# Kernel optimization log

Hardware: AMD Instinct MI355X
Metric: run time of the kernel (lower is better)

## Reference

```python
import jax, jax.numpy as jnp
import numpy as np

BS, VARNUM, EMB_DIM, SEED_DIM, N_HEADS = 32, 16384, 128, 128, 16


def setup_inputs() -> dict:
    key = jax.random.key(0)
    k1, k2, k3, k4 = jax.random.split(key, 4)
    query_seed = jax.random.normal(k1, (BS, SEED_DIM), dtype=jnp.float32)
    embeddings = jax.random.normal(k2, (BS, VARNUM, EMB_DIM), dtype=jnp.float32)
    # mask over varnum//2 base variables; 1 = keep, 0 = mask out
    attn_mask = jax.random.randint(k3, (BS, VARNUM // 2), 0, 2, dtype=jnp.int32)
    # xavier_normal_ init: std = sqrt(2 / (fan_in + fan_out))
    xavier_std = float(np.sqrt(2.0 / (EMB_DIM + SEED_DIM)))
    w_qs = jax.random.normal(k4, (N_HEADS, EMB_DIM, SEED_DIM), dtype=jnp.float32) * xavier_std
    return {"query_seed": query_seed, "embeddings": embeddings,
            "attn_mask": attn_mask, "w_qs": w_qs}


def _l2_normalize(x):
    # x / ||x||_2 along last dim (no eps, matching torch source)
    return x / jnp.linalg.norm(x, axis=-1, keepdims=True)


def reference(query_seed, embeddings, attn_mask, w_qs):
    bs, varnum, emb_dim = embeddings.shape
    n_heads = w_qs.shape[0]

    norm_embs = _l2_normalize(embeddings)                      # [bs, varnum, emb]
    # mm(w_qs.view(-1, seed), seed.T).T.view(bs, n_heads, emb) == einsum
    qs = jnp.tanh(jnp.einsum("hes,bs->bhe", w_qs, query_seed))  # [bs, heads, emb]
    norm_qs = _l2_normalize(qs)

    # orthogonality loss between head queries
    gram = jnp.einsum("bhe,bge->bhg", norm_qs, norm_qs)        # [bs, h, h]
    diff = gram - jnp.eye(n_heads, dtype=gram.dtype)
    loss = jnp.sum(diff * diff) / bs

    # cosine-similarity attention
    attn = jnp.einsum("bhe,bve->bhv", norm_qs, norm_embs)      # [bs, h, varnum]
    mask_full = jnp.concatenate([attn_mask, attn_mask], axis=1)[:, None, :]  # [bs,1,varnum]
    attn = jnp.where(mask_full == 0, -jnp.inf, attn)
    final_attn = jax.nn.softmax(attn, axis=-1)
    rc = jnp.einsum("bhv,bve->bhe", final_attn, embeddings)    # values = embeddings
    return rc, loss
```

## Files before the change

### kernel.cpp

```cpp
#include <hip/hip_runtime.h>
#include <hip/hip_bf16.h>
#include <cstdint>

#define BS     32
#define VARNUM 16384
#define EMB    128
#define SEEDD  128
#define NH     16
#define HALFV  8192

#define NCHUNK 32
#define VT     (VARNUM / NCHUNK)
#define TV     64
#define NTILE  (VT / TV)

#define EST 2080
#define PST 144

#define OFF_NORMQ 0
#define SZ_NORMQ  (BS*NH*EMB*4)
#define OFF_LOSSP (OFF_NORMQ + SZ_NORMQ)
#define SZ_LOSSP  256
#define OFF_LPART (OFF_LOSSP + SZ_LOSSP)
#define SZ_LPART  (BS*NCHUNK*NH*4)
#define OFF_PACC  (OFF_LPART + SZ_LPART)
#define SZ_PACC   ((size_t)BS*NCHUNK*NH*EMB*4)

typedef __attribute__((ext_vector_type(8))) short bf16x8;
typedef __attribute__((ext_vector_type(4))) float f32x4;

static __device__ __forceinline__ uint16_t f2bf(float f) {
    uint32_t u = __float_as_uint(f);
    return (uint16_t)((u + 0x7FFFu + ((u >> 16) & 1u)) >> 16);
}
static __device__ __forceinline__ uint32_t packbf(float a, float b) {
    __hip_bfloat162 h = __float22bfloat162_rn(make_float2(a, b));
    uint32_t u;
    __builtin_memcpy(&u, &h, 4);
    return u;
}
static __device__ __forceinline__ float dot4(float4 a, float4 b) {
    return a.x*b.x + a.y*b.y + a.z*b.z + a.w*b.w;
}

__global__ __launch_bounds__(128) void k1_q(const float* __restrict__ seed,
                                            const float* __restrict__ wqs,
                                            float* __restrict__ normq) {
    const int bh = blockIdx.x;
    const int b = bh >> 4, h = bh & 15;
    const int e = threadIdx.x;
    __shared__ __align__(16) float s_seed[SEEDD];
    s_seed[e] = seed[b*SEEDD + e];
    __syncthreads();
    const float4* w4 = (const float4*)(wqs + ((size_t)(h*EMB + e))*SEEDD);
    const float4* s4 = (const float4*)s_seed;
    float acc = 0.f;
    #pragma unroll
    for (int j = 0; j < SEEDD/4; ++j) acc += dot4(w4[j], s4[j]);
    float t = tanhf(acc);
    float sq = t*t;
    #pragma unroll
    for (int off = 32; off; off >>= 1) sq += __shfl_xor(sq, off);
    __shared__ float s_part[2];
    if ((threadIdx.x & 63) == 0) s_part[threadIdx.x >> 6] = sq;
    __syncthreads();
    float tot = s_part[0] + s_part[1];
    normq[((size_t)b*NH + h)*EMB + e] = t * rsqrtf(tot);
}

__global__ __launch_bounds__(256) void k2_loss(const float* __restrict__ normq,
                                               float* __restrict__ lossp) {
    const int b = blockIdx.x;
    const int h = threadIdx.x >> 4, g = threadIdx.x & 15;
    const float4* qh = (const float4*)(normq + ((size_t)b*NH + h)*EMB);
    const float4* qg = (const float4*)(normq + ((size_t)b*NH + g)*EMB);
    float d = 0.f;
    #pragma unroll
    for (int j = 0; j < EMB/4; ++j) d += dot4(qh[j], qg[j]);
    d -= (h == g) ? 1.f : 0.f;
    float sq = d*d;
    #pragma unroll
    for (int off = 32; off; off >>= 1) sq += __shfl_xor(sq, off);
    __shared__ float sp[4];
    if ((threadIdx.x & 63) == 0) sp[threadIdx.x >> 6] = sq;
    __syncthreads();
    if (threadIdx.x == 0) lossp[b] = sp[0] + sp[1] + sp[2] + sp[3];
}

__global__ __launch_bounds__(256, 4) void k_fused(const float* __restrict__ emb,
                                                  const int* __restrict__ mask,
                                                  const float* __restrict__ normq,
                                                  float* __restrict__ pacc,
                                                  float* __restrict__ lpart) {
    const int chunk = blockIdx.x, b = blockIdx.y;
    const int tid = threadIdx.x;
    const int w   = tid >> 6;
    const int l   = tid & 63;
    const int lhi = l >> 4;
    const int llo = l & 15;

    __shared__ __align__(16) unsigned char Elds[8*EST];
    __shared__ __align__(16) unsigned char Plds[16*PST];
    __shared__ __align__(16) float nsq[TV];
    __shared__ float lred[4][NH];

    bf16x8 qf[4];
    {
        const float* qrow = normq + ((size_t)b*NH + llo)*EMB;
        #pragma unroll
        for (int f = 0; f < 4; ++f) {
            const float4* qs = (const float4*)(qrow + f*32 + lhi*8);
            float4 a = qs[0], c = qs[1];
            bf16x8 t;
            t[0]=(short)f2bf(a.x); t[1]=(short)f2bf(a.y); t[2]=(short)f2bf(a.z); t[3]=(short)f2bf(a.w);
            t[4]=(short)f2bf(c.x); t[5]=(short)f2bf(c.y); t[6]=(short)f2bf(c.z); t[7]=(short)f2bf(c.w);
            qf[f] = t;
        }
    }

    f32x4 acc0 = {0.f,0.f,0.f,0.f};
    f32x4 acc1 = {0.f,0.f,0.f,0.f};
    float Lh = 0.f;

    const float* embB  = emb + (size_t)b*VARNUM*EMB;
    const int*   maskB = mask + b*HALFV;
    const int    r0    = tid >> 4;
    const int    cb    = tid & 15;

    int    mk[4];
    float4 pfa[4], pfb[4];
    {
        const int vg00 = chunk*VT;
        #pragma unroll
        for (int rep = 0; rep < 4; ++rep)
            mk[rep] = maskB[(vg00 + rep*16 + r0) & (HALFV-1)];
        #pragma unroll
        for (int rep = 0; rep < 4; ++rep) {
            const int vg = vg00 + rep*16 + r0;
            const float4* src = (const float4*)(embB + (size_t)(mk[rep] ? vg : vg00)*EMB + cb*8);
            pfa[rep] = src[0]; pfb[rep] = src[1];
        }
    }

    for (int t = 0; t < NTILE; ++t) {
        const int vg0  = chunk*VT + t*TV;
        const int vg0n = vg0 + TV;

        int mkn[4];
        if (t + 1 < NTILE) {
            #pragma unroll
            for (int rep = 0; rep < 4; ++rep)
                mkn[rep] = maskB[(vg0n + rep*16 + r0) & (HALFV-1)];
        }

        #pragma unroll
        for (int rep = 0; rep < 4; ++rep) {
            const int row = rep*16 + r0;
            float4 x0 = pfa[rep], x1 = pfb[rep];
            float sq = dot4(x0,x0) + dot4(x1,x1);
            sq += __shfl_xor(sq, 1); sq += __shfl_xor(sq, 2);
            sq += __shfl_xor(sq, 4); sq += __shfl_xor(sq, 8);
            if (cb == 0) nsq[row] = mk[rep] ? sq : 0.f;
            uint32_t d0 = packbf(x0.x, x0.y), d1 = packbf(x0.z, x0.w);
            uint32_t d2 = packbf(x1.x, x1.y), d3 = packbf(x1.z, x1.w);
            *(uint4*)(Elds + (cb>>1)*EST + row*32 + (cb&1)*16) = make_uint4(d0,d1,d2,d3);
        }
        __syncthreads();

        if (t + 1 < NTILE) {
            #pragma unroll
            for (int rep = 0; rep < 4; ++rep) {
                const int vg = vg0n + rep*16 + r0;
                const float4* src = (const float4*)(embB + (size_t)(mkn[rep] ? vg : vg0n)*EMB + cb*8);
                pfa[rep] = src[0]; pfb[rep] = src[1];
                mk[rep]  = mkn[rep];
            }
        }

        f32x4 s = {0.f,0.f,0.f,0.f};
        #pragma unroll
        for (int f = 0; f < 4; ++f) {
            const int eblk = 2*f + (lhi >> 1);
            bf16x8 a = *(const bf16x8*)(Elds + eblk*EST + (w*16 + llo)*32 + (lhi&1)*16);
            s = __builtin_amdgcn_mfma_f32_16x16x32_bf16(a, qf[f], s, 0, 0, 0);
        }
        f32x4 nn = *(const f32x4*)(&nsq[w*16 + lhi*4]);
        float p[4];
        #pragma unroll
        for (int r = 0; r < 4; ++r)
            p[r] = (nn[r] > 0.f) ? __expf(s[r]*rsqrtf(nn[r]) - 1.f) : 0.f;
        uint32_t u0 = packbf(p[0], p[1]), u1 = packbf(p[2], p[3]);
        Lh += __uint_as_float(u0 << 16) + __uint_as_float(u0 & 0xFFFF0000u)
            + __uint_as_float(u1 << 16) + __uint_as_float(u1 & 0xFFFF0000u);
        {
            unsigned char* pdst = Plds + llo*PST + (w*16 + lhi*4)*2;
            *(uint32_t*)(pdst)     = u0;
            *(uint32_t*)(pdst + 4) = u1;
        }
        __syncthreads();

        #pragma unroll
        for (int kf = 0; kf < 2; ++kf) {
            bf16x8 pa = *(const bf16x8*)(Plds + llo*PST + kf*64 + lhi*16);
            #pragma unroll
            for (int et = 0; et < 2; ++et) {
                const unsigned char* base = Elds + (w*2 + et)*EST + llo*2;
                bf16x8 bb;
                #pragma unroll
                for (int i = 0; i < 8; ++i)
                    bb[i] = *(const short*)(base + (size_t)(kf*32 + lhi*8 + i)*32);
                if (et == 0) acc0 = __builtin_amdgcn_mfma_f32_16x16x32_bf16(pa, bb, acc0, 0, 0, 0);
                else         acc1 = __builtin_amdgcn_mfma_f32_16x16x32_bf16(pa, bb, acc1, 0, 0, 0);
            }
        }
        __syncthreads();
    }

    float* pout = pacc + (((size_t)b*NCHUNK + chunk)*NH)*EMB;
    #pragma unroll
    for (int r = 0; r < 4; ++r) {
        pout[(lhi*4 + r)*EMB + w*32 + llo]      = acc0[r];
        pout[(lhi*4 + r)*EMB + w*32 + 16 + llo] = acc1[r];
    }
    Lh += __shfl_xor(Lh, 16);
    Lh += __shfl_xor(Lh, 32);
    if (l < 16) lred[w][l] = Lh;
    __syncthreads();
    if (tid < 16)
        lpart[((size_t)b*NCHUNK + chunk)*NH + tid] =
            lred[0][tid] + lred[1][tid] + lred[2][tid] + lred[3][tid];
}

__global__ __launch_bounds__(128) void k6_out(const float* __restrict__ pacc,
                                              const float* __restrict__ lpart,
                                              float* __restrict__ out) {
    const int bh = blockIdx.x;
    const int b = bh >> 4, h = bh & 15;
    const int e = threadIdx.x;
    float L = 0.f;
    #pragma unroll
    for (int c = 0; c < NCHUNK; ++c) L += lpart[((size_t)b*NCHUNK + c)*NH + h];
    float acc = 0.f;
    for (int k = 0; k < NCHUNK; ++k)
        acc += pacc[(((size_t)b*NCHUNK + k)*NH + h)*EMB + e];
    out[((size_t)b*NH + h)*EMB + e] = acc / L;
}

__global__ __launch_bounds__(64) void k_loss(const float* __restrict__ lossp,
                                             float* __restrict__ out) {
    const int l = threadIdx.x;
    float v = (l < BS) ? lossp[l] : 0.f;
    #pragma unroll
    for (int off = 32; off; off >>= 1) v += __shfl_xor(v, off);
    if (l == 0) out[BS*NH*EMB] = v / (float)BS;
}

extern "C" void kernel_launch(void* const* d_in, const int* in_sizes, int n_in,
                              void* d_out, int out_size, void* d_ws, size_t ws_size,
                              hipStream_t stream) {
    const float* seed = (const float*)d_in[0];
    const float* emb  = (const float*)d_in[1];
    const int*   mask = (const int*)d_in[2];
    const float* wqs  = (const float*)d_in[3];
    float* out = (float*)d_out;

    char* ws = (char*)d_ws;
    float* normq = (float*)(ws + OFF_NORMQ);
    float* lossp = (float*)(ws + OFF_LOSSP);
    float* lpart = (float*)(ws + OFF_LPART);
    float* pacc  = (float*)(ws + OFF_PACC);

    k1_q<<<BS*NH, 128, 0, stream>>>(seed, wqs, normq);
    k2_loss<<<BS, 256, 0, stream>>>(normq, lossp);
    k_fused<<<dim3(NCHUNK, BS), 256, 0, stream>>>(emb, mask, normq, pacc, lpart);
    k6_out<<<BS*NH, 128, 0, stream>>>(pacc, lpart, out);
    k_loss<<<1, 64, 0, stream>>>(lossp, out);
}
```

Measured before the change: 53.53 us.

## Double-buffer embedding LDS tile, use lightweight barriers, fold loss reduction into output kernel

Splits the embedding LDS staging into two buffers so the trailing barrier at the end of each tile iteration can be removed. Swaps __syncthreads for a barrier that waits only on LDS counters (lgkmcnt), so in-flight global prefetch loads are not drained at each barrier. Merges the tiny loss-reduction kernel into the output kernel to save one launch. The cost is twice the LDS footprint for the embedding tile, which may reduce occupancy. Correctness also now depends on the barrier placement across the two buffers, since nsq and Plds are still single-buffered.

```diff
diff --git a/kernel.cpp b/kernel.cpp
--- a/kernel.cpp
+++ b/kernel.cpp
@@ -28,6 +28,11 @@
 
 typedef __attribute__((ext_vector_type(8))) short bf16x8;
 typedef __attribute__((ext_vector_type(4))) float f32x4;
+
+#define BAR() do { \
+    asm volatile("s_waitcnt lgkmcnt(0)" ::: "memory"); \
+    __builtin_amdgcn_s_barrier(); \
+} while (0)
 
 static __device__ __forceinline__ uint16_t f2bf(float f) {
     uint32_t u = __float_as_uint(f);
@@ -99,7 +104,7 @@
     const int lhi = l >> 4;
     const int llo = l & 15;
 
-    __shared__ __align__(16) unsigned char Elds[8*EST];
+    __shared__ __align__(16) unsigned char Elds[2][8*EST];
     __shared__ __align__(16) unsigned char Plds[16*PST];
     __shared__ __align__(16) float nsq[TV];
     __shared__ float lred[4][NH];
@@ -143,8 +148,8 @@
     }
 
     for (int t = 0; t < NTILE; ++t) {
-        const int vg0  = chunk*VT + t*TV;
-        const int vg0n = vg0 + TV;
+        const int vg0n = chunk*VT + (t+1)*TV;
+        unsigned char* Ebuf = Elds[t & 1];
 
         int mkn[4];
         if (t + 1 < NTILE) {
@@ -163,9 +168,8 @@
             if (cb == 0) nsq[row] = mk[rep] ? sq : 0.f;
             uint32_t d0 = packbf(x0.x, x0.y), d1 = packbf(x0.z, x0.w);
             uint32_t d2 = packbf(x1.x, x1.y), d3 = packbf(x1.z, x1.w);
-            *(uint4*)(Elds + (cb>>1)*EST + row*32 + (cb&1)*16) = make_uint4(d0,d1,d2,d3);
-        }
-        __syncthreads();
+            *(uint4*)(Ebuf + (cb>>1)*EST + row*32 + (cb&1)*16) = make_uint4(d0,d1,d2,d3);
+        }
 
         if (t + 1 < NTILE) {
             #pragma unroll
@@ -176,12 +180,13 @@
                 mk[rep]  = mkn[rep];
             }
         }
+        BAR();
 
         f32x4 s = {0.f,0.f,0.f,0.f};
         #pragma unroll
         for (int f = 0; f < 4; ++f) {
             const int eblk = 2*f + (lhi >> 1);
-            bf16x8 a = *(const bf16x8*)(Elds + eblk*EST + (w*16 + llo)*32 + (lhi&1)*16);
+            bf16x8 a = *(const bf16x8*)(Ebuf + eblk*EST + (w*16 + llo)*32 + (lhi&1)*16);
             s = __builtin_amdgcn_mfma_f32_16x16x32_bf16(a, qf[f], s, 0, 0, 0);
         }
         f32x4 nn = *(const f32x4*)(&nsq[w*16 + lhi*4]);
@@ -197,14 +202,14 @@
             *(uint32_t*)(pdst)     = u0;
             *(uint32_t*)(pdst + 4) = u1;
         }
-        __syncthreads();
+        BAR();
 
         #pragma unroll
         for (int kf = 0; kf < 2; ++kf) {
             bf16x8 pa = *(const bf16x8*)(Plds + llo*PST + kf*64 + lhi*16);
             #pragma unroll
             for (int et = 0; et < 2; ++et) {
-                const unsigned char* base = Elds + (w*2 + et)*EST + llo*2;
+                const unsigned char* base = Ebuf + (w*2 + et)*EST + llo*2;
                 bf16x8 bb;
                 #pragma unroll
                 for (int i = 0; i < 8; ++i)
@@ -213,7 +218,6 @@
                 else         acc1 = __builtin_amdgcn_mfma_f32_16x16x32_bf16(pa, bb, acc1, 0, 0, 0);
             }
         }
-        __syncthreads();
     }
 
     float* pout = pacc + (((size_t)b*NCHUNK + chunk)*NH)*EMB;
@@ -225,7 +229,7 @@
     Lh += __shfl_xor(Lh, 16);
     Lh += __shfl_xor(Lh, 32);
     if (l < 16) lred[w][l] = Lh;
-    __syncthreads();
+    BAR();
     if (tid < 16)
         lpart[((size_t)b*NCHUNK + chunk)*NH + tid] =
             lred[0][tid] + lred[1][tid] + lred[2][tid] + lred[3][tid];
@@ -233,6 +237,7 @@
 
 __global__ __launch_bounds__(128) void k6_out(const float* __restrict__ pacc,
                                               const float* __restrict__ lpart,
+                                              const float* __restrict__ lossp,
                                               float* __restrict__ out) {
     const int bh = blockIdx.x;
     const int b = bh >> 4, h = bh & 15;
@@ -244,15 +249,12 @@
     for (int k = 0; k < NCHUNK; ++k)
         acc += pacc[(((size_t)b*NCHUNK + k)*NH + h)*EMB + e];
     out[((size_t)b*NH + h)*EMB + e] = acc / L;
-}
-
-__global__ __launch_bounds__(64) void k_loss(const float* __restrict__ lossp,
-                                             float* __restrict__ out) {
-    const int l = threadIdx.x;
-    float v = (l < BS) ? lossp[l] : 0.f;
-    #pragma unroll
-    for (int off = 32; off; off >>= 1) v += __shfl_xor(v, off);
-    if (l == 0) out[BS*NH*EMB] = v / (float)BS;
+    if (bh == 0 && e < 64) {
+        float v = (e < BS) ? lossp[e] : 0.f;
+        #pragma unroll
+        for (int off = 32; off; off >>= 1) v += __shfl_xor(v, off);
+        if (e == 0) out[BS*NH*EMB] = v / (float)BS;
+    }
 }
 
 extern "C" void kernel_launch(void* const* d_in, const int* in_sizes, int n_in,
@@ -273,6 +275,5 @@
     k1_q<<<BS*NH, 128, 0, stream>>>(seed, wqs, normq);
     k2_loss<<<BS, 256, 0, stream>>>(normq, lossp);
     k_fused<<<dim3(NCHUNK, BS), 256, 0, stream>>>(emb, mask, normq, pacc, lpart);
-    k6_out<<<BS*NH, 128, 0, stream>>>(pacc, lpart, out);
-    k_loss<<<1, 64, 0, stream>>>(lossp, out);
-}
+    k6_out<<<BS*NH, 128, 0, stream>>>(pacc, lpart, lossp, out);
+}
```

Result: faster. 51.13 us (-4.5%).
